# Optimization experiments

Hardware: AMD Instinct MI355X
Metric: run time of the kernel (lower is better)

The kernel has to match this reference:

```python
import jax, jax.numpy as jnp
import numpy as np

K = 3
STRIDE = 1
PAD = 1


def _conv2d(x, w, b):
    y = jax.lax.conv_general_dilated(
        x, w, window_strides=(STRIDE, STRIDE),
        padding=[(PAD, PAD), (PAD, PAD)],
        dimension_numbers=("NCHW", "OIHW", "NCHW"))
    return y + b[None, :, None, None]


def _bilinear_sample(xb, py, px):
    # xb: [C, H, W]; py, px: [K2, Ho, Wo] float sample coords
    C, H, W = xb.shape
    y0 = jnp.floor(py)
    x0 = jnp.floor(px)
    ay = py - y0  # frac weights
    ax = px - x0
    out = jnp.zeros((C,) + py.shape, dtype=xb.dtype)
    corners = [
        (y0, x0, (1.0 - ay) * (1.0 - ax)),
        (y0, x0 + 1.0, (1.0 - ay) * ax),
        (y0 + 1.0, x0, ay * (1.0 - ax)),
        (y0 + 1.0, x0 + 1.0, ay * ax),
    ]
    for yc, xc, wgt in corners:
        valid = (yc >= 0) & (yc < H) & (xc >= 0) & (xc < W)
        yi = jnp.clip(yc, 0, H - 1).astype(jnp.int32)
        xi = jnp.clip(xc, 0, W - 1).astype(jnp.int32)
        g = xb[:, yi, xi]  # [C, K2, Ho, Wo]
        out = out + g * (wgt * valid.astype(xb.dtype))[None]
    return out


def _deform_forward(x, weight, bias, p_weight, p_bias):
    B, Cin, H, W = x.shape
    Cout = weight.shape[0]
    K2 = K * K
    # offset / mask prediction conv
    pout = _conv2d(x, p_weight, p_bias)  # [B, 3*K2, Ho, Wo]
    o1, o2, m = jnp.split(pout, 3, axis=1)
    offset = jnp.concatenate([o1, o2], axis=1)  # [B, 2*K2, Ho, Wo]
    mask = jax.nn.sigmoid(m)  # [B, K2, Ho, Wo]
    Ho, Wo = mask.shape[2], mask.shape[3]
    # torchvision layout: channel 2k = dy_k, 2k+1 = dx_k
    off = offset.reshape(B, K2, 2, Ho, Wo)
    dy, dx = off[:, :, 0], off[:, :, 1]  # [B, K2, Ho, Wo]
    ki = (jnp.arange(K2) // K).astype(x.dtype)  # kernel row
    kj = (jnp.arange(K2) % K).astype(x.dtype)   # kernel col
    base_y = jnp.arange(Ho, dtype=x.dtype) * STRIDE - PAD  # [Ho]
    base_x = jnp.arange(Wo, dtype=x.dtype) * STRIDE - PAD  # [Wo]
    py = base_y[None, None, :, None] + ki[None, :, None, None] + dy
    px = base_x[None, None, None, :] + kj[None, :, None, None] + dx
    sampled = jax.vmap(_bilinear_sample)(x, py, px)  # [B, Cin, K2, Ho, Wo]
    sampled = sampled * mask[:, None]
    w = weight.reshape(Cout, Cin, K2)
    out = jnp.einsum('bckhw,ock->bohw', sampled, w) + bias[None, :, None, None]
    return out


def setup_inputs() -> dict:
    key = jax.random.key(0)
    k1, k2, k3 = jax.random.split(key, 3)
    B, Cin, Cout, H, W = 4, 256, 256, 64, 64
    x = jax.random.normal(k1, (B, Cin, H, W), dtype=jnp.float32)
    fan_in = Cin * K * K
    weight = jax.random.normal(k2, (Cout, Cin, K, K), dtype=jnp.float32) / np.sqrt(fan_in)
    bias = jnp.zeros((Cout,), dtype=jnp.float32)
    # small random offset/mask predictor (zero-init in the original; randomized
    # here so the deformable sampling path is exercised)
    p_weight = jax.random.normal(k3, (3 * K * K, Cin, K, K), dtype=jnp.float32) * 0.02
    p_bias = jnp.zeros((3 * K * K,), dtype=jnp.float32)
    return {"x": x, "weight": weight, "bias": bias, "p_weight": p_weight, "p_bias": p_bias}


def reference(x, weight, bias, p_weight, p_bias):
    return _deform_forward(x, weight, bias, p_weight, p_bias)
```

## Files before the change

### kernel.cpp

```cpp
#include <hip/hip_runtime.h>
#include <stdint.h>


#define CIN 256
#define COUT 256
#define HWS 4096
#define MTOT 16384
#define KTOT 2304
#define SPLITK 8

typedef __attribute__((ext_vector_type(8))) short bf16x8;
typedef __attribute__((ext_vector_type(4))) float f32x4;

__device__ __forceinline__ unsigned short f2bf(float f) {
  unsigned int u = __float_as_uint(f);
  unsigned int r = (u + 0x7fffu + ((u >> 16) & 1u)) >> 16;
  return (unsigned short)r;
}
__device__ __forceinline__ float bf2f(unsigned short u) {
  return __uint_as_float(((unsigned int)u) << 16);
}
__device__ __forceinline__ float bflo(unsigned int u) { return __uint_as_float(u << 16); }
__device__ __forceinline__ float bfhi(unsigned int u) { return __uint_as_float(u & 0xffff0000u); }

__device__ __forceinline__ void gload_lds16(const void* g, void* l) {
  __builtin_amdgcn_global_load_lds((const __attribute__((address_space(1))) void*)g,
                                   (__attribute__((address_space(3))) void*)l, 16, 0, 0);
}

#define GLOAD16(D, P) asm volatile("global_load_dwordx4 %0, %1, off" : "=v"(D) : "v"(P))
#define WAITVM(N)                                            \
  {                                                          \
    asm volatile("s_waitcnt vmcnt(" #N ")" ::: "memory");    \
    __builtin_amdgcn_sched_barrier(0);                       \
  }
#define BARRIER_LGKM                                                  \
  { asm volatile("s_waitcnt lgkmcnt(0)\n\ts_barrier" ::: "memory"); }

#define ASW(c, rr) ((c) ^ (((rr) & 7) << 3))

__global__ __launch_bounds__(256) void prep_and_transpose(const float* __restrict__ x,
                                                          const float* __restrict__ w,
                                                          const float* __restrict__ pw,
                                                          unsigned short* __restrict__ xt,
                                                          unsigned short* __restrict__ WB,
                                                          unsigned short* __restrict__ PWs) {
  __shared__ float tile[64][65];
  int bid = blockIdx.x;
  int tid = threadIdx.x;
  if (bid < 1024) {
    int b = bid >> 8;
    int rest = bid & 255;
    int hw0 = (rest & 63) * 64;
    int c0 = (rest >> 6) * 64;
    {
      int col4 = (tid & 15) * 4;
      int crow = tid >> 4;
#pragma unroll
      for (int it = 0; it < 4; ++it) {
        int c = it * 16 + crow;
        float4 v = *(const float4*)&x[(size_t)(b * CIN + c0 + c) * HWS + hw0 + col4];
        tile[c][col4] = v.x;
        tile[c][col4 + 1] = v.y;
        tile[c][col4 + 2] = v.z;
        tile[c][col4 + 3] = v.w;
      }
    }
    __syncthreads();
    {
      int cc0 = (tid & 7) * 8;
      int rrow = tid >> 3;
#pragma unroll
      for (int it = 0; it < 2; ++it) {
        int r = it * 32 + rrow;
        uint4 o;
        o.x = (unsigned)f2bf(tile[cc0][r])     | ((unsigned)f2bf(tile[cc0 + 1][r]) << 16);
        o.y = (unsigned)f2bf(tile[cc0 + 2][r]) | ((unsigned)f2bf(tile[cc0 + 3][r]) << 16);
        o.z = (unsigned)f2bf(tile[cc0 + 4][r]) | ((unsigned)f2bf(tile[cc0 + 5][r]) << 16);
        o.w = (unsigned)f2bf(tile[cc0 + 6][r]) | ((unsigned)f2bf(tile[cc0 + 7][r]) << 16);
        *(uint4*)&xt[(size_t)(b * HWS + hw0 + r) * CIN + c0 + cc0] = o;
      }
    }
  } else {
    int idx = (bid - 1024) * 256 + tid;
    if (idx < KTOT * COUT) {
      int f = idx;
      int e = f & 7;
      int row = (f >> 3) & 15;
      int quad = (f >> 7) & 3;
      int j = (f >> 9) & 15;
      int t = f >> 13;
      int kk = t * 32 + quad * 8 + e;
      int o = j * 16 + row;
      int k = kk >> 8, c = kk & 255;
      WB[f] = f2bf(w[o * KTOT + c * 9 + k]);
    } else {
      int f2 = idx - KTOT * COUT;
      int t_ = f2 & 7;
      int rest = f2 >> 3;
      int j = rest & 31;
      int kk = (rest >> 5) * 8 + t_;
      int k = kk >> 8, c = kk & 255;
      float v = (j < 27) ? pw[j * KTOT + c * 9 + k] : 0.0f;
      PWs[f2] = f2bf(v);
    }
  }
}

__device__ __forceinline__ void bilin8p(const uint4 c00, const uint4 c01,
                                        const uint4 c10, const uint4 c11,
                                        const float4 w4, unsigned short* dst) {
  uint4 o;
  float v0, v1;
  v0 = w4.x * bflo(c00.x) + w4.y * bflo(c01.x) + w4.z * bflo(c10.x) + w4.w * bflo(c11.x);
  v1 = w4.x * bfhi(c00.x) + w4.y * bfhi(c01.x) + w4.z * bfhi(c10.x) + w4.w * bfhi(c11.x);
  o.x = (unsigned)f2bf(v0) | ((unsigned)f2bf(v1) << 16);
  v0 = w4.x * bflo(c00.y) + w4.y * bflo(c01.y) + w4.z * bflo(c10.y) + w4.w * bflo(c11.y);
  v1 = w4.x * bfhi(c00.y) + w4.y * bfhi(c01.y) + w4.z * bfhi(c10.y) + w4.w * bfhi(c11.y);
  o.y = (unsigned)f2bf(v0) | ((unsigned)f2bf(v1) << 16);
  v0 = w4.x * bflo(c00.z) + w4.y * bflo(c01.z) + w4.z * bflo(c10.z) + w4.w * bflo(c11.z);
  v1 = w4.x * bfhi(c00.z) + w4.y * bfhi(c01.z) + w4.z * bfhi(c10.z) + w4.w * bfhi(c11.z);
  o.z = (unsigned)f2bf(v0) | ((unsigned)f2bf(v1) << 16);
  v0 = w4.x * bflo(c00.w) + w4.y * bflo(c01.w) + w4.z * bflo(c10.w) + w4.w * bflo(c11.w);
  v1 = w4.x * bfhi(c00.w) + w4.y * bfhi(c01.w) + w4.z * bfhi(c10.w) + w4.w * bfhi(c11.w);
  o.w = (unsigned)f2bf(v0) | ((unsigned)f2bf(v1) << 16);
  *(uint4*)dst = o;
}

#define MFMA16P(B0, B1, B2, B3)                                                          \
  acc[0][0] = __builtin_amdgcn_mfma_f32_16x16x32_bf16(afr0, B0, acc[0][0], 0, 0, 0);     \
  acc[0][1] = __builtin_amdgcn_mfma_f32_16x16x32_bf16(afr0, B1, acc[0][1], 0, 0, 0);     \
  acc[1][0] = __builtin_amdgcn_mfma_f32_16x16x32_bf16(afr1, B0, acc[1][0], 0, 0, 0);     \
  acc[1][1] = __builtin_amdgcn_mfma_f32_16x16x32_bf16(afr1, B1, acc[1][1], 0, 0, 0);     \
  acc[2][0] = __builtin_amdgcn_mfma_f32_16x16x32_bf16(afr2, B0, acc[2][0], 0, 0, 0);     \
  acc[2][1] = __builtin_amdgcn_mfma_f32_16x16x32_bf16(afr2, B1, acc[2][1], 0, 0, 0);     \
  acc[3][0] = __builtin_amdgcn_mfma_f32_16x16x32_bf16(afr3, B0, acc[3][0], 0, 0, 0);     \
  acc[3][1] = __builtin_amdgcn_mfma_f32_16x16x32_bf16(afr3, B1, acc[3][1], 0, 0, 0);     \
  acc[0][0] = __builtin_amdgcn_mfma_f32_16x16x32_bf16(afr4, B2, acc[0][0], 0, 0, 0);     \
  acc[0][1] = __builtin_amdgcn_mfma_f32_16x16x32_bf16(afr4, B3, acc[0][1], 0, 0, 0);     \
  acc[1][0] = __builtin_amdgcn_mfma_f32_16x16x32_bf16(afr5, B2, acc[1][0], 0, 0, 0);     \
  acc[1][1] = __builtin_amdgcn_mfma_f32_16x16x32_bf16(afr5, B3, acc[1][1], 0, 0, 0);     \
  acc[2][0] = __builtin_amdgcn_mfma_f32_16x16x32_bf16(afr6, B2, acc[2][0], 0, 0, 0);     \
  acc[2][1] = __builtin_amdgcn_mfma_f32_16x16x32_bf16(afr6, B3, acc[2][1], 0, 0, 0);     \
  acc[3][0] = __builtin_amdgcn_mfma_f32_16x16x32_bf16(afr7, B2, acc[3][0], 0, 0, 0);     \
  acc[3][1] = __builtin_amdgcn_mfma_f32_16x16x32_bf16(afr7, B3, acc[3][1], 0, 0, 0);

#define FITER_P2(P, PAR, GI0, GI1, GI2, GI3, GC0, GC1, GC2, GC3,                         \
                 BC0, BC1, BC2, BC3, BI0, BI1, BI2, BI3)                                 \
  {                                                                                      \
    const unsigned short* btn = bpb + (size_t)(2 * ((P) + 1)) * 8192;                    \
    GLOAD16(BI0, btn);                                                                   \
    GLOAD16(BI1, btn + 512);                                                             \
    GLOAD16(BI2, btn + 8192);                                                            \
    GLOAD16(BI3, btn + 8192 + 512);                                                      \
    if ((((P) + 2) & 3) == 0) dI4 = Tbl[r][((P) + 2) >> 2][0];                           \
    int cb = ((2 * (P) + 4) & 7) * 32 + qo8;                                             \
    GLOAD16(GI0, xtb + dI4.x + cb);                                                      \
    GLOAD16(GI1, xtb + dI4.y + cb);                                                      \
    GLOAD16(GI2, xtb + dI4.z + cb);                                                      \
    GLOAD16(GI3, xtb + dI4.w + cb);                                                      \
    afr0 = *(const bf16x8*)&As[PAR][row][ASW(quad * 8, row)];                            \
    afr1 = *(const bf16x8*)&As[PAR][16 + row][ASW(quad * 8, row)];                       \
    afr2 = *(const bf16x8*)&As[PAR][32 + row][ASW(quad * 8, row)];                       \
    afr3 = *(const bf16x8*)&As[PAR][48 + row][ASW(quad * 8, row)];                       \
    afr4 = *(const bf16x8*)&As[PAR][row][ASW(32 + quad * 8, row)];                       \
    afr5 = *(const bf16x8*)&As[PAR][16 + row][ASW(32 + quad * 8, row)];                  \
    afr6 = *(const bf16x8*)&As[PAR][32 + row][ASW(32 + quad * 8, row)];                  \
    afr7 = *(const bf16x8*)&As[PAR][48 + row][ASW(32 + quad * 8, row)];                  \
    if ((((P) + 1) & 3) == 0) dW4 = *(float4*)&Tbl[r][((P) + 1) >> 2][1];                \
    WAITVM(12)                                                                           \
    MFMA16P(BC0, BC1, BC2, BC3)                                                          \
    WAITVM(8)                                                                            \
    bilin8p(GC0, GC1, GC2, GC3, dW4, &As[PAR ^ 1][r][ASW(qo8, r)]);                      \
    BARRIER_LGKM                                                                         \
  }

__global__ __launch_bounds__(512, 2) void fused_gemm(const unsigned short* __restrict__ xt,
                                                     const unsigned short* __restrict__ PWs,
                                                     const float* __restrict__ p_bias,
                                                     const unsigned short* __restrict__ WB,
                                                     const float* __restrict__ bias,
                                                     float* __restrict__ out) {
  __shared__ unsigned short As[2][64][64];
  __shared__ int4 Tbl[64][9][2];
  __shared__ float Ptl[8][64][32];

  int tid = threadIdx.x;
  int lane = tid & 63, wv = tid >> 6;
  int row = lane & 15, quad = lane >> 4;
  int mt = (blockIdx.x & 7) * 32 + (blockIdx.x >> 3);
  int mb = mt * 64;
  int b = mb >> 12;
  int hw0 = mb & 4095;
  const unsigned short* xtb = xt + ((size_t)b << 20);

  {
    f32x4 aco[4][2] = {};
    for (int tt = 0; tt < 9; ++tt) {
      int t = wv * 9 + tt;
      int k = t >> 3, c0 = (t & 7) * 32;
      int dyk = k / 3 - 1, dxk = k % 3 - 1;
      const unsigned short* pb = PWs + (size_t)t * 1024 + (quad * 32 + row) * 8;
      bf16x8 ob0 = *(const bf16x8*)pb;
      bf16x8 ob1 = *(const bf16x8*)(pb + 128);
#pragma unroll
      for (int rs = 0; rs < 4; ++rs) {
        int hw = hw0 + rs * 16 + row;
        int h = hw >> 6, wq = hw & 63;
        int y = h + dyk, xx = wq + dxk;
        bf16x8 oa = {};
        if (((unsigned)y < 64u) && ((unsigned)xx < 64u))
          oa = *(const bf16x8*)(xtb + (size_t)(((y << 6) + xx) << 8) + c0 + quad * 8);
        aco[rs][0] = __builtin_amdgcn_mfma_f32_16x16x32_bf16(oa, ob0, aco[rs][0], 0, 0, 0);
        aco[rs][1] = __builtin_amdgcn_mfma_f32_16x16x32_bf16(oa, ob1, aco[rs][1], 0, 0, 0);
      }
    }
#pragma unroll
    for (int rs = 0; rs < 4; ++rs)
#pragma unroll
      for (int j = 0; j < 2; ++j)
#pragma unroll
        for (int e = 0; e < 4; ++e)
          Ptl[wv][rs * 16 + quad * 4 + e][j * 16 + row] = aco[rs][j][e];
  }
  __syncthreads();

  for (int i = tid; i < 2048; i += 512) {
    int lm = i >> 5, n = i & 31;
    float s = Ptl[0][lm][n];
#pragma unroll
    for (int w = 1; w < 8; ++w) s += Ptl[w][lm][n];
    Ptl[0][lm][n] = s;
  }
  __syncthreads();

  for (int pr = tid; pr < 576; pr += 512) {
    int lm = pr / 9;
    int k = pr - lm * 9;
    int m = mb + lm;

    float dy = p_bias[2 * k] + Ptl[0][lm][2 * k];
    float dx = p_bias[2 * k + 1] + Ptl[0][lm][2 * k + 1];
    float mv = p_bias[18 + k] + Ptl[0][lm][18 + k];
    float mk = 1.0f / (1.0f + __expf(-mv));

    int hw = m & 4095, h = hw >> 6, ww = hw & 63;
    float py = (float)(h - 1 + k / 3) + dy;
    float px = (float)(ww - 1 + k % 3) + dx;
    float y0f = floorf(py), x0f = floorf(px);
    float ay = py - y0f, ax = px - x0f;
    int y0 = (int)y0f, x0 = (int)x0f;

    float w00 = (1.f - ay) * (1.f - ax) * mk;
    float w01 = (1.f - ay) * ax * mk;
    float w10 = ay * (1.f - ax) * mk;
    float w11 = ay * ax * mk;

    float vy0 = ((unsigned)y0 < 64u) ? 1.f : 0.f;
    float vy1 = ((unsigned)(y0 + 1) < 64u) ? 1.f : 0.f;
    float vx0 = ((unsigned)x0 < 64u) ? 1.f : 0.f;
    float vx1 = ((unsigned)(x0 + 1) < 64u) ? 1.f : 0.f;
    w00 *= vy0 * vx0; w01 *= vy0 * vx1; w10 *= vy1 * vx0; w11 *= vy1 * vx1;

    int yc0 = min(max(y0, 0), 63), yc1 = min(max(y0 + 1, 0), 63);
    int xc0 = min(max(x0, 0), 63), xc1 = min(max(x0 + 1, 0), 63);

    Tbl[lm][k][0] = make_int4((yc0 * 64 + xc0) * 256, (yc0 * 64 + xc1) * 256,
                              (yc1 * 64 + xc0) * 256, (yc1 * 64 + xc1) * 256);
    *(float4*)&Tbl[lm][k][1] = make_float4(w00, w01, w10, w11);
  }
  __syncthreads();

  int r = tid >> 3;
  int qo8 = (tid & 7) * 8;

  int4 dI4 = Tbl[r][0][0];
  float4 dW4 = *(float4*)&Tbl[r][0][1];

  const unsigned short* bpb = WB + (size_t)(wv * 2) * 512 + quad * 128 + row * 8;

  f32x4 acc[4][2] = {};
  uint4 gA0, gA1, gA2, gA3;
  uint4 gB0, gB1, gB2, gB3;
  bf16x8 bA0, bA1, bA2, bA3;
  bf16x8 bB0, bB1, bB2, bB3;
  bf16x8 afr0, afr1, afr2, afr3, afr4, afr5, afr6, afr7;

  {
    uint4 p00 = *(const uint4*)(xtb + dI4.x + qo8);
    uint4 p01 = *(const uint4*)(xtb + dI4.y + qo8);
    uint4 p10 = *(const uint4*)(xtb + dI4.z + qo8);
    uint4 p11 = *(const uint4*)(xtb + dI4.w + qo8);
    bilin8p(p00, p01, p10, p11, dW4, &As[0][r][ASW(qo8, r)]);
    GLOAD16(bA0, bpb);
    GLOAD16(bA1, bpb + 512);
    GLOAD16(bA2, bpb + 8192);
    GLOAD16(bA3, bpb + 8192 + 512);
    int cb1 = 64 + qo8;
    GLOAD16(gA0, xtb + dI4.x + cb1);
    GLOAD16(gA1, xtb + dI4.y + cb1);
    GLOAD16(gA2, xtb + dI4.z + cb1);
    GLOAD16(gA3, xtb + dI4.w + cb1);
  }
  BARRIER_LGKM

#pragma unroll 1
  for (int p = 0; p < 34; p += 2) {
    FITER_P2(p,     0, gB0, gB1, gB2, gB3, gA0, gA1, gA2, gA3,
                       bA0, bA1, bA2, bA3, bB0, bB1, bB2, bB3)
    FITER_P2(p + 1, 1, gA0, gA1, gA2, gA3, gB0, gB1, gB2, gB3,
                       bB0, bB1, bB2, bB3, bA0, bA1, bA2, bA3)
  }

  {
    const unsigned short* btn = bpb + (size_t)70 * 8192;
    GLOAD16(bB0, btn);
    GLOAD16(bB1, btn + 512);
    GLOAD16(bB2, btn + 8192);
    GLOAD16(bB3, btn + 8192 + 512);
    afr0 = *(const bf16x8*)&As[0][row][ASW(quad * 8, row)];
    afr1 = *(const bf16x8*)&As[0][16 + row][ASW(quad * 8, row)];
    afr2 = *(const bf16x8*)&As[0][32 + row][ASW(quad * 8, row)];
    afr3 = *(const bf16x8*)&As[0][48 + row][ASW(quad * 8, row)];
    afr4 = *(const bf16x8*)&As[0][row][ASW(32 + quad * 8, row)];
    afr5 = *(const bf16x8*)&As[0][16 + row][ASW(32 + quad * 8, row)];
    afr6 = *(const bf16x8*)&As[0][32 + row][ASW(32 + quad * 8, row)];
    afr7 = *(const bf16x8*)&As[0][48 + row][ASW(32 + quad * 8, row)];
    WAITVM(8)
    MFMA16P(bA0, bA1, bA2, bA3)
    WAITVM(4)
    bilin8p(gA0, gA1, gA2, gA3, dW4, &As[1][r][ASW(qo8, r)]);
    BARRIER_LGKM
  }
  {
    afr0 = *(const bf16x8*)&As[1][row][ASW(quad * 8, row)];
    afr1 = *(const bf16x8*)&As[1][16 + row][ASW(quad * 8, row)];
    afr2 = *(const bf16x8*)&As[1][32 + row][ASW(quad * 8, row)];
    afr3 = *(const bf16x8*)&As[1][48 + row][ASW(quad * 8, row)];
    afr4 = *(const bf16x8*)&As[1][row][ASW(32 + quad * 8, row)];
    afr5 = *(const bf16x8*)&As[1][16 + row][ASW(32 + quad * 8, row)];
    afr6 = *(const bf16x8*)&As[1][32 + row][ASW(32 + quad * 8, row)];
    afr7 = *(const bf16x8*)&As[1][48 + row][ASW(32 + quad * 8, row)];
    WAITVM(0)
    MFMA16P(bB0, bB1, bB2, bB3)
  }

#pragma unroll
  for (int j = 0; j < 2; ++j) {
    int o = wv * 32 + j * 16 + row;
    float bo = bias[o];
#pragma unroll
    for (int i = 0; i < 4; ++i) {
      int hw = hw0 + i * 16 + quad * 4;
      float4 v;
      v.x = acc[i][j][0] + bo;
      v.y = acc[i][j][1] + bo;
      v.z = acc[i][j][2] + bo;
      v.w = acc[i][j][3] + bo;
      *(float4*)(out + (((size_t)(b * COUT + o)) << 12) + hw) = v;
    }
  }
}

extern "C" void kernel_launch(void* const* d_in, const int* in_sizes, int n_in,
                              void* d_out, int out_size, void* d_ws, size_t ws_size,
                              hipStream_t stream) {
  const float* x        = (const float*)d_in[0];
  const float* weight   = (const float*)d_in[1];
  const float* bias     = (const float*)d_in[2];
  const float* p_weight = (const float*)d_in[3];
  const float* p_bias   = (const float*)d_in[4];
  float* out = (float*)d_out;
  char* ws = (char*)d_ws;

  const size_t OFF_XT   = 0;
  const size_t OFF_WB   = OFF_XT + 8388608;
  const size_t OFF_PW   = OFF_WB + 1179648;

  unsigned short* xt    = (unsigned short*)(ws + OFF_XT);
  unsigned short* WB    = (unsigned short*)(ws + OFF_WB);
  unsigned short* PWs   = (unsigned short*)(ws + OFF_PW);

  prep_and_transpose<<<1024 + 2592, 256, 0, stream>>>(x, weight, p_weight, xt, WB, PWs);
  fused_gemm<<<256, 512, 0, stream>>>(xt, PWs, p_bias, WB, bias, out);
}
```

Measured before the change: 123.7 us.

## Double fused_gemm block to 1024 threads, halving per-wave output tile and gather width

```diff
diff --git a/kernel.cpp b/kernel.cpp
--- a/kernel.cpp
+++ b/kernel.cpp
@@ -29,6 +29,7 @@
 }
 
 #define GLOAD16(D, P) asm volatile("global_load_dwordx4 %0, %1, off" : "=v"(D) : "v"(P))
+#define GLOAD8(D, P)  asm volatile("global_load_dwordx2 %0, %1, off" : "=v"(D) : "v"(P))
 #define WAITVM(N)                                            \
   {                                                          \
     asm volatile("s_waitcnt vmcnt(" #N ")" ::: "memory");    \
@@ -107,10 +108,10 @@
   }
 }
 
-__device__ __forceinline__ void bilin8p(const uint4 c00, const uint4 c01,
-                                        const uint4 c10, const uint4 c11,
+__device__ __forceinline__ void bilin4p(const uint2 c00, const uint2 c01,
+                                        const uint2 c10, const uint2 c11,
                                         const float4 w4, unsigned short* dst) {
-  uint4 o;
+  uint2 o;
   float v0, v1;
   v0 = w4.x * bflo(c00.x) + w4.y * bflo(c01.x) + w4.z * bflo(c10.x) + w4.w * bflo(c11.x);
   v1 = w4.x * bfhi(c00.x) + w4.y * bfhi(c01.x) + w4.z * bfhi(c10.x) + w4.w * bfhi(c11.x);
@@ -118,47 +119,30 @@
   v0 = w4.x * bflo(c00.y) + w4.y * bflo(c01.y) + w4.z * bflo(c10.y) + w4.w * bflo(c11.y);
   v1 = w4.x * bfhi(c00.y) + w4.y * bfhi(c01.y) + w4.z * bfhi(c10.y) + w4.w * bfhi(c11.y);
   o.y = (unsigned)f2bf(v0) | ((unsigned)f2bf(v1) << 16);
-  v0 = w4.x * bflo(c00.z) + w4.y * bflo(c01.z) + w4.z * bflo(c10.z) + w4.w * bflo(c11.z);
-  v1 = w4.x * bfhi(c00.z) + w4.y * bfhi(c01.z) + w4.z * bfhi(c10.z) + w4.w * bfhi(c11.z);
-  o.z = (unsigned)f2bf(v0) | ((unsigned)f2bf(v1) << 16);
-  v0 = w4.x * bflo(c00.w) + w4.y * bflo(c01.w) + w4.z * bflo(c10.w) + w4.w * bflo(c11.w);
-  v1 = w4.x * bfhi(c00.w) + w4.y * bfhi(c01.w) + w4.z * bfhi(c10.w) + w4.w * bfhi(c11.w);
-  o.w = (unsigned)f2bf(v0) | ((unsigned)f2bf(v1) << 16);
-  *(uint4*)dst = o;
-}
-
-#define MFMA16P(B0, B1, B2, B3)                                                          \
-  acc[0][0] = __builtin_amdgcn_mfma_f32_16x16x32_bf16(afr0, B0, acc[0][0], 0, 0, 0);     \
-  acc[0][1] = __builtin_amdgcn_mfma_f32_16x16x32_bf16(afr0, B1, acc[0][1], 0, 0, 0);     \
-  acc[1][0] = __builtin_amdgcn_mfma_f32_16x16x32_bf16(afr1, B0, acc[1][0], 0, 0, 0);     \
-  acc[1][1] = __builtin_amdgcn_mfma_f32_16x16x32_bf16(afr1, B1, acc[1][1], 0, 0, 0);     \
-  acc[2][0] = __builtin_amdgcn_mfma_f32_16x16x32_bf16(afr2, B0, acc[2][0], 0, 0, 0);     \
-  acc[2][1] = __builtin_amdgcn_mfma_f32_16x16x32_bf16(afr2, B1, acc[2][1], 0, 0, 0);     \
-  acc[3][0] = __builtin_amdgcn_mfma_f32_16x16x32_bf16(afr3, B0, acc[3][0], 0, 0, 0);     \
-  acc[3][1] = __builtin_amdgcn_mfma_f32_16x16x32_bf16(afr3, B1, acc[3][1], 0, 0, 0);     \
-  acc[0][0] = __builtin_amdgcn_mfma_f32_16x16x32_bf16(afr4, B2, acc[0][0], 0, 0, 0);     \
-  acc[0][1] = __builtin_amdgcn_mfma_f32_16x16x32_bf16(afr4, B3, acc[0][1], 0, 0, 0);     \
-  acc[1][0] = __builtin_amdgcn_mfma_f32_16x16x32_bf16(afr5, B2, acc[1][0], 0, 0, 0);     \
-  acc[1][1] = __builtin_amdgcn_mfma_f32_16x16x32_bf16(afr5, B3, acc[1][1], 0, 0, 0);     \
-  acc[2][0] = __builtin_amdgcn_mfma_f32_16x16x32_bf16(afr6, B2, acc[2][0], 0, 0, 0);     \
-  acc[2][1] = __builtin_amdgcn_mfma_f32_16x16x32_bf16(afr6, B3, acc[2][1], 0, 0, 0);     \
-  acc[3][0] = __builtin_amdgcn_mfma_f32_16x16x32_bf16(afr7, B2, acc[3][0], 0, 0, 0);     \
-  acc[3][1] = __builtin_amdgcn_mfma_f32_16x16x32_bf16(afr7, B3, acc[3][1], 0, 0, 0);
-
-#define FITER_P2(P, PAR, GI0, GI1, GI2, GI3, GC0, GC1, GC2, GC3,                         \
-                 BC0, BC1, BC2, BC3, BI0, BI1, BI2, BI3)                                 \
+  *(uint2*)dst = o;
+}
+
+#define MFMA8X(B0, B1)                                                                   \
+  acc[0] = __builtin_amdgcn_mfma_f32_16x16x32_bf16(afr0, B0, acc[0], 0, 0, 0);           \
+  acc[1] = __builtin_amdgcn_mfma_f32_16x16x32_bf16(afr1, B0, acc[1], 0, 0, 0);           \
+  acc[2] = __builtin_amdgcn_mfma_f32_16x16x32_bf16(afr2, B0, acc[2], 0, 0, 0);           \
+  acc[3] = __builtin_amdgcn_mfma_f32_16x16x32_bf16(afr3, B0, acc[3], 0, 0, 0);           \
+  acc[0] = __builtin_amdgcn_mfma_f32_16x16x32_bf16(afr4, B1, acc[0], 0, 0, 0);           \
+  acc[1] = __builtin_amdgcn_mfma_f32_16x16x32_bf16(afr5, B1, acc[1], 0, 0, 0);           \
+  acc[2] = __builtin_amdgcn_mfma_f32_16x16x32_bf16(afr6, B1, acc[2], 0, 0, 0);           \
+  acc[3] = __builtin_amdgcn_mfma_f32_16x16x32_bf16(afr7, B1, acc[3], 0, 0, 0);
+
+#define FITER_P3(P, PAR, GI0, GI1, GI2, GI3, GC0, GC1, GC2, GC3, BC0, BC1, BI0, BI1)     \
   {                                                                                      \
     const unsigned short* btn = bpb + (size_t)(2 * ((P) + 1)) * 8192;                    \
     GLOAD16(BI0, btn);                                                                   \
-    GLOAD16(BI1, btn + 512);                                                             \
-    GLOAD16(BI2, btn + 8192);                                                            \
-    GLOAD16(BI3, btn + 8192 + 512);                                                      \
+    GLOAD16(BI1, btn + 8192);                                                            \
     if ((((P) + 2) & 3) == 0) dI4 = Tbl[r][((P) + 2) >> 2][0];                           \
-    int cb = ((2 * (P) + 4) & 7) * 32 + qo8;                                             \
-    GLOAD16(GI0, xtb + dI4.x + cb);                                                      \
-    GLOAD16(GI1, xtb + dI4.y + cb);                                                      \
-    GLOAD16(GI2, xtb + dI4.z + cb);                                                      \
-    GLOAD16(GI3, xtb + dI4.w + cb);                                                      \
+    int cb = ((2 * (P) + 4) & 7) * 32 + go;                                              \
+    GLOAD8(GI0, xtb + dI4.x + cb);                                                       \
+    GLOAD8(GI1, xtb + dI4.y + cb);                                                       \
+    GLOAD8(GI2, xtb + dI4.z + cb);                                                       \
+    GLOAD8(GI3, xtb + dI4.w + cb);                                                       \
     afr0 = *(const bf16x8*)&As[PAR][row][ASW(quad * 8, row)];                            \
     afr1 = *(const bf16x8*)&As[PAR][16 + row][ASW(quad * 8, row)];                       \
     afr2 = *(const bf16x8*)&As[PAR][32 + row][ASW(quad * 8, row)];                       \
@@ -168,19 +152,19 @@
     afr6 = *(const bf16x8*)&As[PAR][32 + row][ASW(32 + quad * 8, row)];                  \
     afr7 = *(const bf16x8*)&As[PAR][48 + row][ASW(32 + quad * 8, row)];                  \
     if ((((P) + 1) & 3) == 0) dW4 = *(float4*)&Tbl[r][((P) + 1) >> 2][1];                \
-    WAITVM(12)                                                                           \
-    MFMA16P(BC0, BC1, BC2, BC3)                                                          \
-    WAITVM(8)                                                                            \
-    bilin8p(GC0, GC1, GC2, GC3, dW4, &As[PAR ^ 1][r][ASW(qo8, r)]);                      \
+    WAITVM(10)                                                                           \
+    MFMA8X(BC0, BC1)                                                                     \
+    WAITVM(6)                                                                            \
+    bilin4p(GC0, GC1, GC2, GC3, dW4, &As[PAR ^ 1][r][ASW(go, r)]);                       \
     BARRIER_LGKM                                                                         \
   }
 
-__global__ __launch_bounds__(512, 2) void fused_gemm(const unsigned short* __restrict__ xt,
-                                                     const unsigned short* __restrict__ PWs,
-                                                     const float* __restrict__ p_bias,
-                                                     const unsigned short* __restrict__ WB,
-                                                     const float* __restrict__ bias,
-                                                     float* __restrict__ out) {
+__global__ __launch_bounds__(1024, 4) void fused_gemm(const unsigned short* __restrict__ xt,
+                                                      const unsigned short* __restrict__ PWs,
+                                                      const float* __restrict__ p_bias,
+                                                      const unsigned short* __restrict__ WB,
+                                                      const float* __restrict__ bias,
+                                                      float* __restrict__ out) {
   __shared__ unsigned short As[2][64][64];
   __shared__ int4 Tbl[64][9][2];
   __shared__ float Ptl[8][64][32];
@@ -194,7 +178,7 @@
   int hw0 = mb & 4095;
   const unsigned short* xtb = xt + ((size_t)b << 20);
 
-  {
+  if (wv < 8) {
     f32x4 aco[4][2] = {};
     for (int tt = 0; tt < 9; ++tt) {
       int t = wv * 9 + tt;
@@ -225,7 +209,7 @@
   }
   __syncthreads();
 
-  for (int i = tid; i < 2048; i += 512) {
+  for (int i = tid; i < 2048; i += 1024) {
     int lm = i >> 5, n = i & 31;
     float s = Ptl[0][lm][n];
 #pragma unroll
@@ -234,7 +218,7 @@
   }
   __syncthreads();
 
-  for (int pr = tid; pr < 576; pr += 512) {
+  for (int pr = tid; pr < 576; pr += 1024) {
     int lm = pr / 9;
     int k = pr - lm * 9;
     int m = mb + lm;
@@ -271,53 +255,47 @@
   }
   __syncthreads();
 
-  int r = tid >> 3;
-  int qo8 = (tid & 7) * 8;
+  int sub = tid & 15;
+  int r = tid >> 4;
+  int go = (sub >> 3) * 32 + (sub & 7) * 4;
 
   int4 dI4 = Tbl[r][0][0];
   float4 dW4 = *(float4*)&Tbl[r][0][1];
 
-  const unsigned short* bpb = WB + (size_t)(wv * 2) * 512 + quad * 128 + row * 8;
-
-  f32x4 acc[4][2] = {};
-  uint4 gA0, gA1, gA2, gA3;
-  uint4 gB0, gB1, gB2, gB3;
-  bf16x8 bA0, bA1, bA2, bA3;
-  bf16x8 bB0, bB1, bB2, bB3;
+  const unsigned short* bpb = WB + (size_t)wv * 512 + quad * 128 + row * 8;
+
+  f32x4 acc[4] = {};
+  uint2 gA0, gA1, gA2, gA3;
+  uint2 gB0, gB1, gB2, gB3;
+  bf16x8 bA0, bA1;
+  bf16x8 bB0, bB1;
   bf16x8 afr0, afr1, afr2, afr3, afr4, afr5, afr6, afr7;
 
   {
-    uint4 p00 = *(const uint4*)(xtb + dI4.x + qo8);
-    uint4 p01 = *(const uint4*)(xtb + dI4.y + qo8);
-    uint4 p10 = *(const uint4*)(xtb + dI4.z + qo8);
-    uint4 p11 = *(const uint4*)(xtb + dI4.w + qo8);
-    bilin8p(p00, p01, p10, p11, dW4, &As[0][r][ASW(qo8, r)]);
+    uint2 p00 = *(const uint2*)(xtb + dI4.x + go);
+    uint2 p01 = *(const uint2*)(xtb + dI4.y + go);
+    uint2 p10 = *(const uint2*)(xtb + dI4.z + go);
+    uint2 p11 = *(const uint2*)(xtb + dI4.w + go);
+    bilin4p(p00, p01, p10, p11, dW4, &As[0][r][ASW(go, r)]);
     GLOAD16(bA0, bpb);
-    GLOAD16(bA1, bpb + 512);
-    GLOAD16(bA2, bpb + 8192);
-    GLOAD16(bA3, bpb + 8192 + 512);
-    int cb1 = 64 + qo8;
-    GLOAD16(gA0, xtb + dI4.x + cb1);
-    GLOAD16(gA1, xtb + dI4.y + cb1);
-    GLOAD16(gA2, xtb + dI4.z + cb1);
-    GLOAD16(gA3, xtb + dI4.w + cb1);
+    GLOAD16(bA1, bpb + 8192);
+    int cb1 = 64 + go;
+    GLOAD8(gA0, xtb + dI4.x + cb1);
+    GLOAD8(gA1, xtb + dI4.y + cb1);
+    GLOAD8(gA2, xtb + dI4.z + cb1);
+    GLOAD8(gA3, xtb + dI4.w + cb1);
   }
   BARRIER_LGKM
 
 #pragma unroll 1
   for (int p = 0; p < 34; p += 2) {
-    FITER_P2(p,     0, gB0, gB1, gB2, gB3, gA0, gA1, gA2, gA3,
-                       bA0, bA1, bA2, bA3, bB0, bB1, bB2, bB3)
-    FITER_P2(p + 1, 1, gA0, gA1, gA2, gA3, gB0, gB1, gB2, gB3,
-                       bB0, bB1, bB2, bB3, bA0, bA1, bA2, bA3)
+    FITER_P3(p,     0, gB0, gB1, gB2, gB3, gA0, gA1, gA2, gA3, bA0, bA1, bB0, bB1)
+    FITER_P3(p + 1, 1, gA0, gA1, gA2, gA3, gB0, gB1, gB2, gB3, bB0, bB1, bA0, bA1)
   }
 
   {
-    const unsigned short* btn = bpb + (size_t)70 * 8192;
-    GLOAD16(bB0, btn);
-    GLOAD16(bB1, btn + 512);
-    GLOAD16(bB2, btn + 8192);
-    GLOAD16(bB3, btn + 8192 + 512);
+    GLOAD16(bB0, bpb + (size_t)70 * 8192);
+    GLOAD16(bB1, bpb + (size_t)71 * 8192);
     afr0 = *(const bf16x8*)&As[0][row][ASW(quad * 8, row)];
     afr1 = *(const bf16x8*)&As[0][16 + row][ASW(quad * 8, row)];
     afr2 = *(const bf16x8*)&As[0][32 + row][ASW(quad * 8, row)];
@@ -326,10 +304,10 @@
     afr5 = *(const bf16x8*)&As[0][16 + row][ASW(32 + quad * 8, row)];
     afr6 = *(const bf16x8*)&As[0][32 + row][ASW(32 + quad * 8, row)];
     afr7 = *(const bf16x8*)&As[0][48 + row][ASW(32 + quad * 8, row)];
-    WAITVM(8)
-    MFMA16P(bA0, bA1, bA2, bA3)
-    WAITVM(4)
-    bilin8p(gA0, gA1, gA2, gA3, dW4, &As[1][r][ASW(qo8, r)]);
+    WAITVM(6)
+    MFMA8X(bA0, bA1)
+    WAITVM(2)
+    bilin4p(gA0, gA1, gA2, gA3, dW4, &As[1][r][ASW(go, r)]);
     BARRIER_LGKM
   }
   {
@@ -342,21 +320,20 @@
     afr6 = *(const bf16x8*)&As[1][32 + row][ASW(32 + quad * 8, row)];
     afr7 = *(const bf16x8*)&As[1][48 + row][ASW(32 + quad * 8, row)];
     WAITVM(0)
-    MFMA16P(bB0, bB1, bB2, bB3)
-  }
-
-#pragma unroll
-  for (int j = 0; j < 2; ++j) {
-    int o = wv * 32 + j * 16 + row;
+    MFMA8X(bB0, bB1)
+  }
+
+  {
+    int o = wv * 16 + row;
     float bo = bias[o];
 #pragma unroll
-    for (int i = 0; i < 4; ++i) {
-      int hw = hw0 + i * 16 + quad * 4;
+    for (int mi = 0; mi < 4; ++mi) {
+      int hw = hw0 + mi * 16 + quad * 4;
       float4 v;
-      v.x = acc[i][j][0] + bo;
-      v.y = acc[i][j][1] + bo;
-      v.z = acc[i][j][2] + bo;
-      v.w = acc[i][j][3] + bo;
+      v.x = acc[mi][0] + bo;
+      v.y = acc[mi][1] + bo;
+      v.z = acc[mi][2] + bo;
+      v.w = acc[mi][3] + bo;
       *(float4*)(out + (((size_t)(b * COUT + o)) << 12) + hw) = v;
     }
   }
@@ -382,5 +359,5 @@
   unsigned short* PWs   = (unsigned short*)(ws + OFF_PW);
 
   prep_and_transpose<<<1024 + 2592, 256, 0, stream>>>(x, weight, p_weight, xt, WB, PWs);
-  fused_gemm<<<256, 512, 0, stream>>>(xt, PWs, p_bias, WB, bias, out);
-}
+  fused_gemm<<<256, 1024, 0, stream>>>(xt, PWs, p_bias, WB, bias, out);
+}
```

Result: slower. 127.9 us (+3.4%).
